# Kernel optimization log

Measured on AMD Instinct MI355X. Metric: run time of the kernel, lower is better.

Reference implementation:

```python
import jax, jax.numpy as jnp
import numpy as np

N, E, F_IN, H, L, G = 50000, 800000, 128, 256, 64, 500


def setup_inputs() -> dict:
    key = jax.random.key(0)
    ks = jax.random.split(key, 12)
    s = 0.02
    x = jax.random.normal(ks[0], (N, F_IN), dtype=jnp.float32)
    edge_index = jax.random.randint(ks[1], (2, E), 0, N, dtype=jnp.int64 if jax.config.jax_enable_x64 else jnp.int32)
    batch = jnp.sort(jax.random.randint(ks[2], (N,), 0, G, dtype=jnp.int32))
    return {
        "x": x,
        "edge_index": edge_index,
        "batch": batch,
        "num_graphs": G,
        "W1": jax.random.normal(ks[3], (F_IN, H), dtype=jnp.float32) * s,
        "b1": jnp.zeros((H,), dtype=jnp.float32),
        "W2": jax.random.normal(ks[4], (H, H), dtype=jnp.float32) * s,
        "b2": jnp.zeros((H,), dtype=jnp.float32),
        "Wmu": jax.random.normal(ks[5], (H, L), dtype=jnp.float32) * s,
        "bmu": jnp.zeros((L,), dtype=jnp.float32),
        "Wlv": jax.random.normal(ks[6], (H, L), dtype=jnp.float32) * s,
        "blv": jnp.zeros((L,), dtype=jnp.float32),
    }


def _gcn_norm(edge_index, n_nodes):
    # PyG GCNConv default: add self-loops, symmetric normalization D^-1/2 A_hat D^-1/2
    loop = jnp.arange(n_nodes, dtype=edge_index.dtype)
    src = jnp.concatenate([edge_index[0], loop])
    dst = jnp.concatenate([edge_index[1], loop])
    deg = jax.ops.segment_sum(jnp.ones_like(dst, dtype=jnp.float32), dst, num_segments=n_nodes)
    dinv = jnp.where(deg > 0, jax.lax.rsqrt(deg), 0.0)
    norm = dinv[src] * dinv[dst]  # [E + N]
    return src, dst, norm


def _gcn_conv(h, src, dst, norm, W, b, n_nodes):
    h = h @ W                              # [N, out]
    msg = norm[:, None] * h[src]           # gather + scale: [E+N, out]
    agg = jax.ops.segment_sum(msg, dst, num_segments=n_nodes)  # scatter-add
    return agg + b


def reference(x, edge_index, batch, num_graphs, W1, b1, W2, b2, Wmu, bmu, Wlv, blv):
    n_nodes = x.shape[0]
    src, dst, norm = _gcn_norm(edge_index, n_nodes)
    h = jax.nn.relu(_gcn_conv(x, src, dst, norm, W1, b1, n_nodes))
    h = jax.nn.relu(_gcn_conv(h, src, dst, norm, W2, b2, n_nodes))
    # global_mean_pool over batch ids
    sums = jax.ops.segment_sum(h, batch, num_segments=num_graphs)       # [G, H]
    cnt = jax.ops.segment_sum(jnp.ones((n_nodes,), h.dtype), batch, num_segments=num_graphs)
    h_graph = sums / jnp.maximum(cnt, 1.0)[:, None]
    mu = h_graph @ Wmu + bmu
    logvar = h_graph @ Wlv + blv
    return mu, logvar
```

## Files before the change

kernel.cpp:

```cpp
#include <hip/hip_runtime.h>
#include <hip/hip_fp16.h>

#define N_NODES 50000
#define N_EDGES 800000
#define F_IN_D  128
#define H_DIM   256
#define L_DIM   64
#define G_NUM   500

typedef unsigned int   u32;
typedef unsigned short u16;
typedef unsigned char  u8;
typedef __attribute__((ext_vector_type(8))) short short8;
typedef __attribute__((ext_vector_type(4))) float f32x4;
typedef __attribute__((ext_vector_type(2))) float f32x2;

#define BSHIFT 8
#define NBUCK ((N_NODES + 255) >> BSHIFT)
#define CUR_STRIDE 16
#define BIN_NB 512
#define EPB ((N_EDGES + BIN_NB - 1) / BIN_NB)
#define BUCK_CAP 8192

static __device__ __forceinline__ float bf2f(u16 u) {
    union { u32 i; float f; } x; x.i = ((u32)u) << 16; return x.f;
}
static __device__ __forceinline__ u16 f2bf(float f) {
    union { float f; u32 i; } x; x.f = f;
    u32 r = (x.i + 0x7fffu + ((x.i >> 16) & 1u)) >> 16;
    return (u16)r;
}
static __device__ __forceinline__ float edge_w(u32 e) {
    return __half2float(__ushort_as_half((u16)(e >> 16)));
}

static __device__ __forceinline__ u32 pack4_fp8(u32 a, u32 b) {
    u32 w = __builtin_amdgcn_cvt_pk_fp8_f32(bf2f((u16)(a & 0xffff)),
                                            bf2f((u16)(a >> 16)), 0, false);
    w = __builtin_amdgcn_cvt_pk_fp8_f32(bf2f((u16)(b & 0xffff)),
                                        bf2f((u16)(b >> 16)), w, true);
    return w;
}

static __device__ __forceinline__ u32 bswz_idx(int n, int k, int plane, int KS) {
    int n0g = n >> 6, nt = (n >> 4) & 3, lr = n & 15;
    int k0i = k >> 5, ks = k & 31, lq = ks >> 3, j = ks & 7;
    return ((u32)((((n0g * KS + k0i) * 2 + plane) * 4 + nt) * 64 + lq * 16 + lr)) * 8 + j;
}

#define NXQ (N_NODES * F_IN_D / 4)
#define NW1 (F_IN_D * H_DIM)
#define NW2 (H_DIM * H_DIM)
#define NB_SCAN  ((N_NODES + 255) / 256)
#define NB_CONV  ((NXQ + NW1 + NW2 + 255) / 256)

__global__ void prep_kernel(const int* __restrict__ batch, int* __restrict__ goff,
                            const float* __restrict__ x, u16* __restrict__ xb,
                            const float* __restrict__ W1, u16* __restrict__ w1swz,
                            const float* __restrict__ W2, u16* __restrict__ w2swz,
                            int* __restrict__ bcur) {
    int b = blockIdx.x;
    if (b < NB_SCAN) {
        int i = b * 256 + threadIdx.x;
        if (i >= N_NODES) return;
        int v = batch[i];
        if (i == 0) {
            for (int g = 0; g <= v; ++g) goff[g] = 0;
        } else {
            int p = batch[i - 1];
            for (int g = p + 1; g <= v; ++g) goff[g] = i;
        }
        if (i == N_NODES - 1) {
            for (int g = v + 1; g <= G_NUM; ++g) goff[g] = N_NODES;
        }
    } else if (b < NB_SCAN + NB_CONV) {
        int i = (b - NB_SCAN) * 256 + threadIdx.x;
        if (i < NXQ) {
            float4 v = *(const float4*)&x[(size_t)i * 4];
            ushort4 o;
            o.x = f2bf(v.x); o.y = f2bf(v.y); o.z = f2bf(v.z); o.w = f2bf(v.w);
            *(ushort4*)&xb[(size_t)i * 4] = o;
        } else if (i < NXQ + NW1) {
            int idx = i - NXQ;
            int k = idx >> 8, n = idx & 255;
            float w = W1[idx];
            u16 h = f2bf(w);
            w1swz[bswz_idx(n, k, 0, F_IN_D / 32)] = h;
            w1swz[bswz_idx(n, k, 1, F_IN_D / 32)] = f2bf(w - bf2f(h));
        } else if (i < NXQ + NW1 + NW2) {
            int idx = i - NXQ - NW1;
            int k = idx >> 8, n = idx & 255;
            float w = W2[idx];
            u16 h = f2bf(w);
            w2swz[bswz_idx(n, k, 0, H_DIM / 32)] = h;
            w2swz[bswz_idx(n, k, 1, H_DIM / 32)] = f2bf(w - bf2f(h));
        }
    } else {
        int t = threadIdx.x;
        if (t < NBUCK) bcur[t * CUR_STRIDE] = t * BUCK_CAP;
    }
}

__global__ void scan_chunk_kernel(const int* __restrict__ in, int* __restrict__ excl,
                                  int* __restrict__ partials, float* __restrict__ dinv, int n) {
    __shared__ int sm[256];
    int t = threadIdx.x;
    int i = blockIdx.x * 256 + t;
    int v = (i < n) ? in[i] : 0;
    sm[t] = v; __syncthreads();
    for (int off = 1; off < 256; off <<= 1) {
        int x = (t >= off) ? sm[t - off] : 0;
        __syncthreads();
        sm[t] += x;
        __syncthreads();
    }
    if (i < n) {
        excl[i] = sm[t] - v;
        dinv[i] = 1.0f / sqrtf((float)(v + 1));
    }
    if (t == 255) partials[blockIdx.x] = sm[255];
}

__global__ void scan_final_kernel(const int* __restrict__ excl, const int* __restrict__ partials,
                                  int* __restrict__ out, int n, int nb) {
    __shared__ int sm[256];
    int t = threadIdx.x;
    int v = (t < nb) ? partials[t] : 0;
    sm[t] = v; __syncthreads();
    for (int off = 1; off < 256; off <<= 1) {
        int x = (t >= off) ? sm[t - off] : 0;
        __syncthreads();
        sm[t] += x;
        __syncthreads();
    }
    int pre = (blockIdx.x > 0) ? sm[blockIdx.x - 1] : 0;
    int i = blockIdx.x * 256 + t;
    if (i < n) out[i] = excl[i] + pre;
    if (blockIdx.x == (unsigned)(nb - 1) && t == 0) out[n] = sm[nb - 1];
}

__global__ __launch_bounds__(256)
void bin_kernel(const int* __restrict__ src, const int* __restrict__ dst,
                int* __restrict__ bcur, u32* __restrict__ binrec) {
    __shared__ int lhist[NBUCK];
    __shared__ int lbase[NBUCK];
    int t = threadIdx.x;
    int e0 = blockIdx.x * EPB;
    int e1 = e0 + EPB; if (e1 > N_EDGES) e1 = N_EDGES;
    for (int i = t; i < NBUCK; i += 256) lhist[i] = 0;
    __syncthreads();
    for (int e = e0 + t; e < e1; e += 256)
        atomicAdd(&lhist[dst[e] >> BSHIFT], 1);
    __syncthreads();
    for (int i = t; i < NBUCK; i += 256) {
        int c = lhist[i];
        lbase[i] = c ? atomicAdd(&bcur[i * CUR_STRIDE], c) : 0;
        lhist[i] = 0;
    }
    __syncthreads();
    for (int e = e0 + t; e < e1; e += 256) {
        int d = dst[e], s = src[e];
        int bkt = d >> BSHIFT;
        int rank = atomicAdd(&lhist[bkt], 1);
        binrec[(size_t)lbase[bkt] + rank] = (u32)s | ((u32)(d & 255) << 16);
    }
}

__global__ __launch_bounds__(256)
void cnt_kernel(const int* __restrict__ bcur, const u32* __restrict__ binrec,
                int* __restrict__ hist) {
    __shared__ int lh[256];
    int b = blockIdx.x;
    int t = threadIdx.x;
    lh[t] = 0;
    __syncthreads();
    int s0 = b * BUCK_CAP;
    int s1 = bcur[b * CUR_STRIDE];
    for (int p = s0 + t; p < s1; p += 256)
        atomicAdd(&lh[(binrec[p] >> 16) & 255], 1);
    __syncthreads();
    int n = (b << BSHIFT) + t;
    if (n < N_NODES) hist[n] = lh[t];
}

__global__ __launch_bounds__(256)
void place2_kernel(const int* __restrict__ rp, const int* __restrict__ bcur,
                   const u32* __restrict__ binrec, const float* __restrict__ dinv,
                   u32* __restrict__ csr) {
    __shared__ int ncur[256];
    int b = blockIdx.x;
    int t = threadIdx.x;
    int n0 = b << BSHIFT;
    int n1 = n0 + 256; if (n1 > N_NODES) n1 = N_NODES;
    if (n0 + t < n1) ncur[t] = rp[n0 + t];
    __syncthreads();
    int s0 = b * BUCK_CAP;
    int s1 = bcur[b * CUR_STRIDE];
    for (int p = s0 + t; p < s1; p += 256) {
        u32 r = binrec[p];
        int s = (int)(r & 0xffff);
        int pos = atomicAdd(&ncur[(r >> 16) & 255], 1);
        u32 w = (u32)__half_as_ushort(__float2half(dinv[s]));
        csr[pos] = (u32)s | (w << 16);
    }
}

__global__ __launch_bounds__(256)
void agg128_kernel(const u16* __restrict__ In, const float* __restrict__ dinv,
                   const int* __restrict__ rp, const u32* __restrict__ csr,
                   u16* __restrict__ Out) {
    int node = blockIdx.x * 4 + (threadIdx.x >> 6);
    int lane = threadIdx.x & 63;
    if (node >= N_NODES) return;
    int c = lane * 2;
    float di = dinv[node];
    int r0 = rp[node], r1 = rp[node + 1];
    u32 sv = *(const u32*)&In[(size_t)node * 128 + c];
    float a0 = di * bf2f((u16)(sv & 0xffff));
    float a1 = di * bf2f((u16)(sv >> 16));
    int j = r0;
    for (; j + 8 <= r1; j += 8) {
        u32 e[8];
        u32 v[8];
#pragma unroll
        for (int q = 0; q < 8; ++q) e[q] = csr[j + q];
#pragma unroll
        for (int q = 0; q < 8; ++q) v[q] = *(const u32*)&In[(size_t)(e[q] & 0xffff) * 128 + c];
#pragma unroll
        for (int q = 0; q < 8; ++q) {
            float w = edge_w(e[q]);
            a0 = fmaf(w, bf2f((u16)(v[q] & 0xffff)), a0);
            a1 = fmaf(w, bf2f((u16)(v[q] >> 16)), a1);
        }
    }
    for (; j + 4 <= r1; j += 4) {
        u32 e[4];
        u32 v[4];
#pragma unroll
        for (int q = 0; q < 4; ++q) e[q] = csr[j + q];
#pragma unroll
        for (int q = 0; q < 4; ++q) v[q] = *(const u32*)&In[(size_t)(e[q] & 0xffff) * 128 + c];
#pragma unroll
        for (int q = 0; q < 4; ++q) {
            float w = edge_w(e[q]);
            a0 = fmaf(w, bf2f((u16)(v[q] & 0xffff)), a0);
            a1 = fmaf(w, bf2f((u16)(v[q] >> 16)), a1);
        }
    }
    for (; j < r1; ++j) {
        u32 e = csr[j];
        u32 v = *(const u32*)&In[(size_t)(e & 0xffff) * 128 + c];
        float w = edge_w(e);
        a0 = fmaf(w, bf2f((u16)(v & 0xffff)), a0);
        a1 = fmaf(w, bf2f((u16)(v >> 16)), a1);
    }
    u32 o = ((u32)f2bf(di * a1) << 16) | (u32)f2bf(di * a0);
    *(u32*)&Out[(size_t)node * 128 + c] = o;
}

__global__ __launch_bounds__(256)
void agg256_fp8_kernel(const u8* __restrict__ In, const float* __restrict__ dinv,
                       const int* __restrict__ rp, const u32* __restrict__ csr,
                       u16* __restrict__ Out) {
    int node = blockIdx.x * 4 + (threadIdx.x >> 6);
    int lane = threadIdx.x & 63;
    if (node >= N_NODES) return;
    int c = lane * 4;
    float di = dinv[node];
    int r0 = rp[node], r1 = rp[node + 1];
    u32 sv = *(const u32*)&In[(size_t)node * 256 + c];
    f32x2 s01 = __builtin_amdgcn_cvt_pk_f32_fp8(sv, false);
    f32x2 s23 = __builtin_amdgcn_cvt_pk_f32_fp8(sv, true);
    float a0 = di * s01.x;
    float a1 = di * s01.y;
    float a2 = di * s23.x;
    float a3 = di * s23.y;
    int j = r0;
    for (; j + 8 <= r1; j += 8) {
        u32 e[8];
        u32 v[8];
#pragma unroll
        for (int q = 0; q < 8; ++q) e[q] = csr[j + q];
#pragma unroll
        for (int q = 0; q < 8; ++q) v[q] = *(const u32*)&In[(size_t)(e[q] & 0xffff) * 256 + c];
#pragma unroll
        for (int q = 0; q < 8; ++q) {
            float w = edge_w(e[q]);
            f32x2 p0 = __builtin_amdgcn_cvt_pk_f32_fp8(v[q], false);
            f32x2 p1 = __builtin_amdgcn_cvt_pk_f32_fp8(v[q], true);
            a0 = fmaf(w, p0.x, a0);
            a1 = fmaf(w, p0.y, a1);
            a2 = fmaf(w, p1.x, a2);
            a3 = fmaf(w, p1.y, a3);
        }
    }
    for (; j + 4 <= r1; j += 4) {
        u32 e[4];
        u32 v[4];
#pragma unroll
        for (int q = 0; q < 4; ++q) e[q] = csr[j + q];
#pragma unroll
        for (int q = 0; q < 4; ++q) v[q] = *(const u32*)&In[(size_t)(e[q] & 0xffff) * 256 + c];
#pragma unroll
        for (int q = 0; q < 4; ++q) {
            float w = edge_w(e[q]);
            f32x2 p0 = __builtin_amdgcn_cvt_pk_f32_fp8(v[q], false);
            f32x2 p1 = __builtin_amdgcn_cvt_pk_f32_fp8(v[q], true);
            a0 = fmaf(w, p0.x, a0);
            a1 = fmaf(w, p0.y, a1);
            a2 = fmaf(w, p1.x, a2);
            a3 = fmaf(w, p1.y, a3);
        }
    }
    for (; j < r1; ++j) {
        u32 e = csr[j];
        u32 v = *(const u32*)&In[(size_t)(e & 0xffff) * 256 + c];
        float w = edge_w(e);
        f32x2 p0 = __builtin_amdgcn_cvt_pk_f32_fp8(v, false);
        f32x2 p1 = __builtin_amdgcn_cvt_pk_f32_fp8(v, true);
        a0 = fmaf(w, p0.x, a0);
        a1 = fmaf(w, p0.y, a1);
        a2 = fmaf(w, p1.x, a2);
        a3 = fmaf(w, p1.y, a3);
    }
    uint2 o;
    o.x = ((u32)f2bf(di * a1) << 16) | (u32)f2bf(di * a0);
    o.y = ((u32)f2bf(di * a3) << 16) | (u32)f2bf(di * a2);
    *(uint2*)&Out[(size_t)node * 256 + c] = o;
}

template<int K>
__global__ __launch_bounds__(256, 3)
void gemm1_kernel(const u16* __restrict__ A, const short8* __restrict__ Bswz,
                  const float* __restrict__ bias, u8* __restrict__ Out, int M) {
    const int KS = K / 32;
    __shared__ u16 cst[64][264];
    int tid  = threadIdx.x;
    int wave = tid >> 6, lane = tid & 63;
    int m0 = blockIdx.x * 64;
    int n0 = wave * 64;
    int lr = lane & 15;
    int lk = (lane >> 4) * 8;

    f32x4 acc[4][4];
#pragma unroll
    for (int i = 0; i < 4; ++i)
#pragma unroll
        for (int j = 0; j < 4; ++j) acc[i][j] = {0.f, 0.f, 0.f, 0.f};

    for (int k0i = 0; k0i < KS; ++k0i) {
        int k0 = k0i * 32;
        short8 a[4], bh[4], bl[4];
#pragma unroll
        for (int mt = 0; mt < 4; ++mt) {
            int m = m0 + mt * 16 + lr;
            if (m > M - 1) m = M - 1;
            a[mt] = *(const short8*)&A[(size_t)m * K + k0 + lk];
        }
        const short8* bp = Bswz + ((size_t)(wave * KS + k0i) * 8) * 64 + lane;
#pragma unroll
        for (int nt = 0; nt < 4; ++nt) {
            bh[nt] = bp[(size_t)nt * 64];
            bl[nt] = bp[(size_t)(4 + nt) * 64];
        }
#pragma unroll
        for (int mt = 0; mt < 4; ++mt)
#pragma unroll
            for (int nt = 0; nt < 4; ++nt) {
                acc[mt][nt] = __builtin_amdgcn_mfma_f32_16x16x32_bf16(a[mt], bh[nt], acc[mt][nt], 0, 0, 0);
                acc[mt][nt] = __builtin_amdgcn_mfma_f32_16x16x32_bf16(a[mt], bl[nt], acc[mt][nt], 0, 0, 0);
            }
    }

#pragma unroll
    for (int mt = 0; mt < 4; ++mt)
#pragma unroll
        for (int nt = 0; nt < 4; ++nt) {
            int col = n0 + nt * 16 + lr;
            float b = bias[col];
#pragma unroll
            for (int r = 0; r < 4; ++r) {
                int row = mt * 16 + (lane >> 4) * 4 + r;
                cst[row][col] = f2bf(fmaxf(acc[mt][nt][r] + b, 0.f));
            }
        }
    __syncthreads();
#pragma unroll
    for (int p = 0; p < 8; ++p) {
        int row = p * 8 + (tid >> 5);
        int c16 = (tid & 31) * 8;
        int m = m0 + row;
        if (m < M) {
            uint4 v = *(const uint4*)&cst[row][c16];
            uint2 o = make_uint2(pack4_fp8(v.x, v.y), pack4_fp8(v.z, v.w));
            *(uint2*)&Out[(size_t)m * 256 + c16] = o;
        }
    }
}

__global__ __launch_bounds__(256, 3)
void gemm2_pool_kernel(const u16* __restrict__ A, const short8* __restrict__ Bswz,
                       const float* __restrict__ bias, const int* __restrict__ batch,
                       float* __restrict__ pooled, int M) {
    const int K = H_DIM, KS = K / 32;
    __shared__ u16 cst[64][264];
    __shared__ int batch_s[64];
    int tid  = threadIdx.x;
    int wave = tid >> 6, lane = tid & 63;
    int m0 = blockIdx.x * 64;
    int n0 = wave * 64;
    int lr = lane & 15;
    int lk = (lane >> 4) * 8;

    f32x4 acc[4][4];
#pragma unroll
    for (int i = 0; i < 4; ++i)
#pragma unroll
        for (int j = 0; j < 4; ++j) acc[i][j] = {0.f, 0.f, 0.f, 0.f};

    for (int k0i = 0; k0i < KS; ++k0i) {
        int k0 = k0i * 32;
        short8 a[4], bh[4], bl[4];
#pragma unroll
        for (int mt = 0; mt < 4; ++mt) {
            int m = m0 + mt * 16 + lr;
            if (m > M - 1) m = M - 1;
            a[mt] = *(const short8*)&A[(size_t)m * K + k0 + lk];
        }
        const short8* bp = Bswz + ((size_t)(wave * KS + k0i) * 8) * 64 + lane;
#pragma unroll
        for (int nt = 0; nt < 4; ++nt) {
            bh[nt] = bp[(size_t)nt * 64];
            bl[nt] = bp[(size_t)(4 + nt) * 64];
        }
#pragma unroll
        for (int mt = 0; mt < 4; ++mt)
#pragma unroll
            for (int nt = 0; nt < 4; ++nt) {
                acc[mt][nt] = __builtin_amdgcn_mfma_f32_16x16x32_bf16(a[mt], bh[nt], acc[mt][nt], 0, 0, 0);
                acc[mt][nt] = __builtin_amdgcn_mfma_f32_16x16x32_bf16(a[mt], bl[nt], acc[mt][nt], 0, 0, 0);
            }
    }

    if (tid < 64) {
        int m = m0 + tid;
        batch_s[tid] = (m < M) ? batch[m] : -1;
    }
#pragma unroll
    for (int mt = 0; mt < 4; ++mt)
#pragma unroll
        for (int nt = 0; nt < 4; ++nt) {
            int col = n0 + nt * 16 + lr;
            float b = bias[col];
#pragma unroll
            for (int r = 0; r < 4; ++r) {
                int row = mt * 16 + (lane >> 4) * 4 + r;
                cst[row][col] = f2bf(fmaxf(acc[mt][nt][r] + b, 0.f));
            }
        }
    __syncthreads();

    int rows = M - m0; if (rows > 64) rows = 64;
    float s = 0.f;
    int gp = batch_s[0];
    for (int r = 0; r < rows; ++r) {
        int g = batch_s[r];
        if (g != gp) {
            atomicAdd(&pooled[(size_t)gp * H_DIM + tid], s);
            s = 0.f;
            gp = g;
        }
        s += bf2f(cst[r][tid]);
    }
    atomicAdd(&pooled[(size_t)gp * H_DIM + tid], s);
}

__global__ void head_kernel(const float* __restrict__ pooled, const int* __restrict__ goff,
                            const float* __restrict__ Wmu, const float* __restrict__ bmu,
                            const float* __restrict__ Wlv, const float* __restrict__ blv,
                            float* __restrict__ out) {
    __shared__ float hg[H_DIM];
    int g = blockIdx.x, l = threadIdx.x;
    float inv = 1.0f / fmaxf((float)(goff[g + 1] - goff[g]), 1.0f);
    for (int k = l; k < H_DIM; k += 64) hg[k] = pooled[(size_t)g * H_DIM + k] * inv;
    __syncthreads();
    float mu = bmu[l], lv = blv[l];
    for (int k = 0; k < H_DIM; ++k) {
        float h = hg[k];
        mu = fmaf(h, Wmu[k * L_DIM + l], mu);
        lv = fmaf(h, Wlv[k * L_DIM + l], lv);
    }
    out[(size_t)g * L_DIM + l] = mu;
    out[(size_t)G_NUM * L_DIM + (size_t)g * L_DIM + l] = lv;
}

extern "C" void kernel_launch(void* const* d_in, const int* in_sizes, int n_in,
                              void* d_out, int out_size, void* d_ws, size_t ws_size,
                              hipStream_t stream) {
    const float* x     = (const float*)d_in[0];
    const int*   ei    = (const int*)  d_in[1];
    const int*   batch = (const int*)  d_in[2];
    const float* W1  = (const float*)d_in[4];
    const float* b1  = (const float*)d_in[5];
    const float* W2  = (const float*)d_in[6];
    const float* b2  = (const float*)d_in[7];
    const float* Wmu = (const float*)d_in[8];
    const float* bmu = (const float*)d_in[9];
    const float* Wlv = (const float*)d_in[10];
    const float* blv = (const float*)d_in[11];
    const int* src = ei;
    const int* dst = ei + N_EDGES;

    char* ws = (char*)d_ws;
    size_t off = 0;
    auto alloc = [&](size_t bytes) -> void* {
        void* p = ws + off;
        off += (bytes + 255) & ~(size_t)255;
        return p;
    };
    float* pooled   = (float*)alloc((size_t)G_NUM * H_DIM * 4);
    int*   hist     = (int*)alloc((size_t)N_NODES * 4);
    float* dinv     = (float*)alloc((size_t)N_NODES * 4);
    int*   row_ptr  = (int*)alloc((size_t)(N_NODES + 1) * 4);
    int*   bcur     = (int*)alloc((size_t)NBUCK * CUR_STRIDE * 4);
    u32*   csr      = (u32*)alloc((size_t)N_EDGES * 4);
    u32*   binrec   = (u32*)alloc((size_t)NBUCK * BUCK_CAP * 4);
    int*   excl     = (int*)alloc((size_t)N_NODES * 4);
    int*   partials = (int*)alloc(256 * 4);
    int*   goff     = (int*)alloc((size_t)(G_NUM + 1) * 4);
    u16*   xb    = (u16*)alloc((size_t)N_NODES * F_IN_D * 2);
    u16*   Xa    = (u16*)alloc((size_t)N_NODES * F_IN_D * 2);
    u8*    H8    = (u8*)alloc((size_t)N_NODES * H_DIM);
    u16*   Ha    = (u16*)alloc((size_t)N_NODES * H_DIM * 2);
    u16*   w1swz = (u16*)alloc((size_t)2 * F_IN_D * H_DIM * 2);
    u16*   w2swz = (u16*)alloc((size_t)2 * H_DIM * H_DIM * 2);
    (void)ws_size; (void)n_in; (void)in_sizes; (void)out_size;

    const int GEMM_NB = (N_NODES + 63) / 64;

    hipMemsetAsync(pooled, 0, (size_t)G_NUM * H_DIM * 4, stream);
    prep_kernel<<<NB_SCAN + NB_CONV + 1, 256, 0, stream>>>(
        batch, goff, x, xb, W1, w1swz, W2, w2swz, bcur);
    bin_kernel<<<BIN_NB, 256, 0, stream>>>(src, dst, bcur, binrec);
    cnt_kernel<<<NBUCK, 256, 0, stream>>>(bcur, binrec, hist);
    scan_chunk_kernel<<<NB_SCAN, 256, 0, stream>>>(hist, excl, partials, dinv, N_NODES);
    scan_final_kernel<<<NB_SCAN, 256, 0, stream>>>(excl, partials, row_ptr, N_NODES, NB_SCAN);
    place2_kernel<<<NBUCK, 256, 0, stream>>>(row_ptr, bcur, binrec, dinv, csr);

    agg128_kernel<<<(N_NODES + 3) / 4, 256, 0, stream>>>(xb, dinv, row_ptr, csr, Xa);
    gemm1_kernel<F_IN_D><<<GEMM_NB, 256, 0, stream>>>(Xa, (const short8*)w1swz, b1, H8, N_NODES);
    agg256_fp8_kernel<<<(N_NODES + 3) / 4, 256, 0, stream>>>(H8, dinv, row_ptr, csr, Ha);
    gemm2_pool_kernel<<<GEMM_NB, 256, 0, stream>>>(Ha, (const short8*)w2swz, b2, batch, pooled, N_NODES);

    head_kernel<<<G_NUM, 64, 0, stream>>>(pooled, goff, Wmu, bmu, Wlv, blv, (float*)d_out);
}
```

Before: 266.3 us.

## Fuse edge binning into prep, merge count+scan, quantize input features to fp8

Binning of edges by destination bucket moves into the prep kernel, with bucket cursors zeroed by an extended memset instead of a separate init block. The per-bucket count kernel is merged with the first scan pass, which removes two launches and the hist buffer. The input features are now stored as fp8 rather than bf16 for the first aggregation, halving the bytes gathered per edge. The fp8 step lowers input precision and may increase error against the reference.

Result: faster. 255.7 us (-4.0%).

```diff
diff --git a/kernel.cpp b/kernel.cpp
--- a/kernel.cpp
+++ b/kernel.cpp
@@ -54,14 +54,38 @@
 #define NB_SCAN  ((N_NODES + 255) / 256)
 #define NB_CONV  ((NXQ + NW1 + NW2 + 255) / 256)
 
-__global__ void prep_kernel(const int* __restrict__ batch, int* __restrict__ goff,
-                            const float* __restrict__ x, u16* __restrict__ xb,
+__global__ void prep_kernel(const int* __restrict__ src, const int* __restrict__ dst,
+                            const int* __restrict__ batch, int* __restrict__ goff,
+                            const float* __restrict__ x, u8* __restrict__ xq,
                             const float* __restrict__ W1, u16* __restrict__ w1swz,
                             const float* __restrict__ W2, u16* __restrict__ w2swz,
-                            int* __restrict__ bcur) {
+                            int* __restrict__ bcur, u32* __restrict__ binrec) {
     int b = blockIdx.x;
-    if (b < NB_SCAN) {
-        int i = b * 256 + threadIdx.x;
+    if (b < BIN_NB) {
+        __shared__ int lhist[NBUCK];
+        __shared__ int lbase[NBUCK];
+        int t = threadIdx.x;
+        int e0 = b * EPB;
+        int e1 = e0 + EPB; if (e1 > N_EDGES) e1 = N_EDGES;
+        for (int i = t; i < NBUCK; i += 256) lhist[i] = 0;
+        __syncthreads();
+        for (int e = e0 + t; e < e1; e += 256)
+            atomicAdd(&lhist[dst[e] >> BSHIFT], 1);
+        __syncthreads();
+        for (int i = t; i < NBUCK; i += 256) {
+            int c = lhist[i];
+            lbase[i] = i * BUCK_CAP + (c ? atomicAdd(&bcur[i * CUR_STRIDE], c) : 0);
+            lhist[i] = 0;
+        }
+        __syncthreads();
+        for (int e = e0 + t; e < e1; e += 256) {
+            int d = dst[e], s = src[e];
+            int bkt = d >> BSHIFT;
+            int rank = atomicAdd(&lhist[bkt], 1);
+            binrec[(size_t)lbase[bkt] + rank] = (u32)s | ((u32)(d & 255) << 16);
+        }
+    } else if (b < BIN_NB + NB_SCAN) {
+        int i = (b - BIN_NB) * 256 + threadIdx.x;
         if (i >= N_NODES) return;
         int v = batch[i];
         if (i == 0) {
@@ -73,13 +97,13 @@
         if (i == N_NODES - 1) {
             for (int g = v + 1; g <= G_NUM; ++g) goff[g] = N_NODES;
         }
-    } else if (b < NB_SCAN + NB_CONV) {
-        int i = (b - NB_SCAN) * 256 + threadIdx.x;
+    } else {
+        int i = (b - BIN_NB - NB_SCAN) * 256 + threadIdx.x;
         if (i < NXQ) {
             float4 v = *(const float4*)&x[(size_t)i * 4];
-            ushort4 o;
-            o.x = f2bf(v.x); o.y = f2bf(v.y); o.z = f2bf(v.z); o.w = f2bf(v.w);
-            *(ushort4*)&xb[(size_t)i * 4] = o;
+            u32 w = __builtin_amdgcn_cvt_pk_fp8_f32(v.x, v.y, 0, false);
+            w = __builtin_amdgcn_cvt_pk_fp8_f32(v.z, v.w, w, true);
+            *(u32*)&xq[(size_t)i * 4] = w;
         } else if (i < NXQ + NW1) {
             int idx = i - NXQ;
             int k = idx >> 8, n = idx & 255;
@@ -95,18 +119,26 @@
             w2swz[bswz_idx(n, k, 0, H_DIM / 32)] = h;
             w2swz[bswz_idx(n, k, 1, H_DIM / 32)] = f2bf(w - bf2f(h));
         }
-    } else {
-        int t = threadIdx.x;
-        if (t < NBUCK) bcur[t * CUR_STRIDE] = t * BUCK_CAP;
-    }
-}
-
-__global__ void scan_chunk_kernel(const int* __restrict__ in, int* __restrict__ excl,
-                                  int* __restrict__ partials, float* __restrict__ dinv, int n) {
+    }
+}
+
+__global__ __launch_bounds__(256)
+void cnt_scan_kernel(const int* __restrict__ bcur, const u32* __restrict__ binrec,
+                     int* __restrict__ excl, int* __restrict__ partials,
+                     float* __restrict__ dinv) {
+    __shared__ int lh[256];
     __shared__ int sm[256];
+    int b = blockIdx.x;
     int t = threadIdx.x;
-    int i = blockIdx.x * 256 + t;
-    int v = (i < n) ? in[i] : 0;
+    lh[t] = 0;
+    __syncthreads();
+    int s0 = b * BUCK_CAP;
+    int s1 = s0 + bcur[b * CUR_STRIDE];
+    for (int p = s0 + t; p < s1; p += 256)
+        atomicAdd(&lh[(binrec[p] >> 16) & 255], 1);
+    __syncthreads();
+    int i = (b << BSHIFT) + t;
+    int v = lh[t];
     sm[t] = v; __syncthreads();
     for (int off = 1; off < 256; off <<= 1) {
         int x = (t >= off) ? sm[t - off] : 0;
@@ -114,11 +146,11 @@
         sm[t] += x;
         __syncthreads();
     }
-    if (i < n) {
+    if (i < N_NODES) {
         excl[i] = sm[t] - v;
         dinv[i] = 1.0f / sqrtf((float)(v + 1));
     }
-    if (t == 255) partials[blockIdx.x] = sm[255];
+    if (t == 255) partials[b] = sm[255];
 }
 
 __global__ void scan_final_kernel(const int* __restrict__ excl, const int* __restrict__ partials,
@@ -137,50 +169,6 @@
     int i = blockIdx.x * 256 + t;
     if (i < n) out[i] = excl[i] + pre;
     if (blockIdx.x == (unsigned)(nb - 1) && t == 0) out[n] = sm[nb - 1];
-}
-
-__global__ __launch_bounds__(256)
-void bin_kernel(const int* __restrict__ src, const int* __restrict__ dst,
-                int* __restrict__ bcur, u32* __restrict__ binrec) {
-    __shared__ int lhist[NBUCK];
-    __shared__ int lbase[NBUCK];
-    int t = threadIdx.x;
-    int e0 = blockIdx.x * EPB;
-    int e1 = e0 + EPB; if (e1 > N_EDGES) e1 = N_EDGES;
-    for (int i = t; i < NBUCK; i += 256) lhist[i] = 0;
-    __syncthreads();
-    for (int e = e0 + t; e < e1; e += 256)
-        atomicAdd(&lhist[dst[e] >> BSHIFT], 1);
-    __syncthreads();
-    for (int i = t; i < NBUCK; i += 256) {
-        int c = lhist[i];
-        lbase[i] = c ? atomicAdd(&bcur[i * CUR_STRIDE], c) : 0;
-        lhist[i] = 0;
-    }
-    __syncthreads();
-    for (int e = e0 + t; e < e1; e += 256) {
-        int d = dst[e], s = src[e];
-        int bkt = d >> BSHIFT;
-        int rank = atomicAdd(&lhist[bkt], 1);
-        binrec[(size_t)lbase[bkt] + rank] = (u32)s | ((u32)(d & 255) << 16);
-    }
-}
-
-__global__ __launch_bounds__(256)
-void cnt_kernel(const int* __restrict__ bcur, const u32* __restrict__ binrec,
-                int* __restrict__ hist) {
-    __shared__ int lh[256];
-    int b = blockIdx.x;
-    int t = threadIdx.x;
-    lh[t] = 0;
-    __syncthreads();
-    int s0 = b * BUCK_CAP;
-    int s1 = bcur[b * CUR_STRIDE];
-    for (int p = s0 + t; p < s1; p += 256)
-        atomicAdd(&lh[(binrec[p] >> 16) & 255], 1);
-    __syncthreads();
-    int n = (b << BSHIFT) + t;
-    if (n < N_NODES) hist[n] = lh[t];
 }
 
 __global__ __launch_bounds__(256)
@@ -195,7 +183,7 @@
     if (n0 + t < n1) ncur[t] = rp[n0 + t];
     __syncthreads();
     int s0 = b * BUCK_CAP;
-    int s1 = bcur[b * CUR_STRIDE];
+    int s1 = s0 + bcur[b * CUR_STRIDE];
     for (int p = s0 + t; p < s1; p += 256) {
         u32 r = binrec[p];
         int s = (int)(r & 0xffff);
@@ -206,18 +194,19 @@
 }
 
 __global__ __launch_bounds__(256)
-void agg128_kernel(const u16* __restrict__ In, const float* __restrict__ dinv,
-                   const int* __restrict__ rp, const u32* __restrict__ csr,
-                   u16* __restrict__ Out) {
+void agg128_fp8_kernel(const u8* __restrict__ In, const float* __restrict__ dinv,
+                       const int* __restrict__ rp, const u32* __restrict__ csr,
+                       u16* __restrict__ Out) {
     int node = blockIdx.x * 4 + (threadIdx.x >> 6);
     int lane = threadIdx.x & 63;
     if (node >= N_NODES) return;
     int c = lane * 2;
     float di = dinv[node];
     int r0 = rp[node], r1 = rp[node + 1];
-    u32 sv = *(const u32*)&In[(size_t)node * 128 + c];
-    float a0 = di * bf2f((u16)(sv & 0xffff));
-    float a1 = di * bf2f((u16)(sv >> 16));
+    u32 sv = *(const u16*)&In[(size_t)node * 128 + c];
+    f32x2 s = __builtin_amdgcn_cvt_pk_f32_fp8(sv, false);
+    float a0 = di * s.x;
+    float a1 = di * s.y;
     int j = r0;
     for (; j + 8 <= r1; j += 8) {
         u32 e[8];
@@ -225,12 +214,13 @@
 #pragma unroll
         for (int q = 0; q < 8; ++q) e[q] = csr[j + q];
 #pragma unroll
-        for (int q = 0; q < 8; ++q) v[q] = *(const u32*)&In[(size_t)(e[q] & 0xffff) * 128 + c];
+        for (int q = 0; q < 8; ++q) v[q] = *(const u16*)&In[(size_t)(e[q] & 0xffff) * 128 + c];
 #pragma unroll
         for (int q = 0; q < 8; ++q) {
             float w = edge_w(e[q]);
-            a0 = fmaf(w, bf2f((u16)(v[q] & 0xffff)), a0);
-            a1 = fmaf(w, bf2f((u16)(v[q] >> 16)), a1);
+            f32x2 p = __builtin_amdgcn_cvt_pk_f32_fp8(v[q], false);
+            a0 = fmaf(w, p.x, a0);
+            a1 = fmaf(w, p.y, a1);
         }
     }
     for (; j + 4 <= r1; j += 4) {
@@ -239,20 +229,22 @@
 #pragma unroll
         for (int q = 0; q < 4; ++q) e[q] = csr[j + q];
 #pragma unroll
-        for (int q = 0; q < 4; ++q) v[q] = *(const u32*)&In[(size_t)(e[q] & 0xffff) * 128 + c];
+        for (int q = 0; q < 4; ++q) v[q] = *(const u16*)&In[(size_t)(e[q] & 0xffff) * 128 + c];
 #pragma unroll
         for (int q = 0; q < 4; ++q) {
             float w = edge_w(e[q]);
-            a0 = fmaf(w, bf2f((u16)(v[q] & 0xffff)), a0);
-            a1 = fmaf(w, bf2f((u16)(v[q] >> 16)), a1);
+            f32x2 p = __builtin_amdgcn_cvt_pk_f32_fp8(v[q], false);
+            a0 = fmaf(w, p.x, a0);
+            a1 = fmaf(w, p.y, a1);
         }
     }
     for (; j < r1; ++j) {
         u32 e = csr[j];
-        u32 v = *(const u32*)&In[(size_t)(e & 0xffff) * 128 + c];
+        u32 v = *(const u16*)&In[(size_t)(e & 0xffff) * 128 + c];
         float w = edge_w(e);
-        a0 = fmaf(w, bf2f((u16)(v & 0xffff)), a0);
-        a1 = fmaf(w, bf2f((u16)(v >> 16)), a1);
+        f32x2 p = __builtin_amdgcn_cvt_pk_f32_fp8(v, false);
+        a0 = fmaf(w, p.x, a0);
+        a1 = fmaf(w, p.y, a1);
     }
     u32 o = ((u32)f2bf(di * a1) << 16) | (u32)f2bf(di * a0);
     *(u32*)&Out[(size_t)node * 128 + c] = o;
@@ -519,16 +511,15 @@
         return p;
     };
     float* pooled   = (float*)alloc((size_t)G_NUM * H_DIM * 4);
-    int*   hist     = (int*)alloc((size_t)N_NODES * 4);
+    int*   bcur     = (int*)alloc((size_t)NBUCK * CUR_STRIDE * 4);
     float* dinv     = (float*)alloc((size_t)N_NODES * 4);
     int*   row_ptr  = (int*)alloc((size_t)(N_NODES + 1) * 4);
-    int*   bcur     = (int*)alloc((size_t)NBUCK * CUR_STRIDE * 4);
     u32*   csr      = (u32*)alloc((size_t)N_EDGES * 4);
     u32*   binrec   = (u32*)alloc((size_t)NBUCK * BUCK_CAP * 4);
     int*   excl     = (int*)alloc((size_t)N_NODES * 4);
     int*   partials = (int*)alloc(256 * 4);
     int*   goff     = (int*)alloc((size_t)(G_NUM + 1) * 4);
-    u16*   xb    = (u16*)alloc((size_t)N_NODES * F_IN_D * 2);
+    u8*    xq    = (u8*)alloc((size_t)N_NODES * F_IN_D);
     u16*   Xa    = (u16*)alloc((size_t)N_NODES * F_IN_D * 2);
     u8*    H8    = (u8*)alloc((size_t)N_NODES * H_DIM);
     u16*   Ha    = (u16*)alloc((size_t)N_NODES * H_DIM * 2);
@@ -537,17 +528,16 @@
     (void)ws_size; (void)n_in; (void)in_sizes; (void)out_size;
 
     const int GEMM_NB = (N_NODES + 63) / 64;
-
-    hipMemsetAsync(pooled, 0, (size_t)G_NUM * H_DIM * 4, stream);
-    prep_kernel<<<NB_SCAN + NB_CONV + 1, 256, 0, stream>>>(
-        batch, goff, x, xb, W1, w1swz, W2, w2swz, bcur);
-    bin_kernel<<<BIN_NB, 256, 0, stream>>>(src, dst, bcur, binrec);
-    cnt_kernel<<<NBUCK, 256, 0, stream>>>(bcur, binrec, hist);
-    scan_chunk_kernel<<<NB_SCAN, 256, 0, stream>>>(hist, excl, partials, dinv, N_NODES);
+    size_t zero_bytes = (size_t)((char*)(bcur + NBUCK * CUR_STRIDE) - (char*)pooled);
+
+    hipMemsetAsync(pooled, 0, zero_bytes, stream);
+    prep_kernel<<<BIN_NB + NB_SCAN + NB_CONV, 256, 0, stream>>>(
+        src, dst, batch, goff, x, xq, W1, w1swz, W2, w2swz, bcur, binrec);
+    cnt_scan_kernel<<<NBUCK, 256, 0, stream>>>(bcur, binrec, excl, partials, dinv);
     scan_final_kernel<<<NB_SCAN, 256, 0, stream>>>(excl, partials, row_ptr, N_NODES, NB_SCAN);
     place2_kernel<<<NBUCK, 256, 0, stream>>>(row_ptr, bcur, binrec, dinv, csr);
 
-    agg128_kernel<<<(N_NODES + 3) / 4, 256, 0, stream>>>(xb, dinv, row_ptr, csr, Xa);
+    agg128_fp8_kernel<<<(N_NODES + 3) / 4, 256, 0, stream>>>(xq, dinv, row_ptr, csr, Xa);
     gemm1_kernel<F_IN_D><<<GEMM_NB, 256, 0, stream>>>(Xa, (const short8*)w1swz, b1, H8, N_NODES);
     agg256_fp8_kernel<<<(N_NODES + 3) / 4, 256, 0, stream>>>(H8, dinv, row_ptr, csr, Ha);
     gemm2_pool_kernel<<<GEMM_NB, 256, 0, stream>>>(Ha, (const short8*)w2swz, b2, batch, pooled, N_NODES);
```
